# Performance work log

Hardware: AMD Instinct MI355X
Metric: run time of the kernel (lower is better)

## Reference

```python
import jax, jax.numpy as jnp
import numpy as np

B, N, DIM, HEADS = 8, 512, 512, 16
MAX_DIST, NG = 128, 32
RBF_STOP = 20.0
EPS = 1e-5


def _ln(x, g, b):
    m = jnp.mean(x, axis=-1, keepdims=True)
    v = jnp.mean((x - m) ** 2, axis=-1, keepdims=True)
    return (x - m) * jax.lax.rsqrt(v + EPS) * g + b


def setup_inputs() -> dict:
    key = jax.random.key(0)
    ks = jax.random.split(key, 12)
    d = DIM
    s = 0.02
    return {
        "x": jax.random.normal(ks[0], (B * N, d), jnp.float32),
        "dist_matrix": jax.random.randint(ks[1], (B, N, N), 0, MAX_DIST, jnp.int32),
        "dist_3d": jax.random.uniform(ks[2], (B, N, N), jnp.float32) * RBF_STOP,
        "norm1_g": jnp.ones((d,), jnp.float32),
        "norm1_b": jnp.zeros((d,), jnp.float32),
        "in_proj_w": jax.random.normal(ks[3], (3 * d, d), jnp.float32) * s,
        "in_proj_b": jnp.zeros((3 * d,), jnp.float32),
        "out_proj_w": jax.random.normal(ks[4], (d, d), jnp.float32) * s,
        "out_proj_b": jnp.zeros((d,), jnp.float32),
        "dist_emb": jax.random.normal(ks[5], (MAX_DIST, HEADS), jnp.float32) * s,
        "rbf_w": jax.random.normal(ks[6], (HEADS, NG), jnp.float32) * s,
        "rbf_b": jnp.zeros((HEADS,), jnp.float32),
        "norm2_g": jnp.ones((d,), jnp.float32),
        "norm2_b": jnp.zeros((d,), jnp.float32),
        "ffn_w1": jax.random.normal(ks[7], (4 * d, d), jnp.float32) * s,
        "ffn_b1": jnp.zeros((4 * d,), jnp.float32),
        "ffn_w2": jax.random.normal(ks[8], (d, 4 * d), jnp.float32) * s,
        "ffn_b2": jnp.zeros((d,), jnp.float32),
        "batch": jnp.repeat(jnp.arange(B, dtype=jnp.int32), N),
    }


def reference(x, dist_matrix, dist_3d, norm1_g, norm1_b, in_proj_w, in_proj_b,
              out_proj_w, out_proj_b, dist_emb, rbf_w, rbf_b, norm2_g, norm2_b,
              ffn_w1, ffn_b1, ffn_w2, ffn_b2, batch):
    b, n = dist_matrix.shape[0], dist_matrix.shape[1]
    d = x.shape[-1]
    dh = d // HEADS
    # equal-size graphs -> to_dense_batch is a reshape, mask all-true
    xd = x.reshape(b, n, d)

    # additive attention bias: shortest-path-distance embedding + RBF projection
    dc = jnp.clip(dist_matrix, 0, MAX_DIST - 1)
    bias_spd = dist_emb[dc]                                  # [b, n, n, H]
    offset = jnp.linspace(0.0, RBF_STOP, NG, dtype=jnp.float32)
    coeff = -0.5 / (RBF_STOP / (NG - 1)) ** 2
    rbf = jnp.exp(coeff * (dist_3d[..., None] - offset) ** 2)  # [b, n, n, NG]
    bias_3d = rbf @ rbf_w.T + rbf_b                          # [b, n, n, H]
    bias = jnp.transpose(bias_spd + bias_3d, (0, 3, 1, 2))   # [b, H, n, n]

    # multi-head attention (pre-norm residual, as in source)
    h = _ln(xd, norm1_g, norm1_b)
    qkv = h @ in_proj_w.T + in_proj_b
    q, k, v = jnp.split(qkv, 3, axis=-1)
    q = q.reshape(b, n, HEADS, dh).transpose(0, 2, 1, 3)
    k = k.reshape(b, n, HEADS, dh).transpose(0, 2, 1, 3)
    v = v.reshape(b, n, HEADS, dh).transpose(0, 2, 1, 3)
    scores = jnp.einsum('bhqd,bhkd->bhqk', q, k) / jnp.sqrt(jnp.float32(dh)) + bias
    attn = jax.nn.softmax(scores, axis=-1)
    ctx = jnp.einsum('bhqk,bhkd->bhqd', attn, v)
    ctx = ctx.transpose(0, 2, 1, 3).reshape(b, n, d)
    attn_out = ctx @ out_proj_w.T + out_proj_b
    h = h + attn_out

    # FFN (dropout inactive at eval)
    h2 = _ln(h, norm2_g, norm2_b)
    ff = jax.nn.gelu(h2 @ ffn_w1.T + ffn_b1, approximate=False) @ ffn_w2.T + ffn_b2
    h = h + ff
    return h.reshape(b * n, d)
```

## Files before the change

### kernel.cpp

```cpp
#include <hip/hip_runtime.h>
#include <hip/hip_bf16.h>
#include <math.h>

#define BB 8
#define NN 512
#define DD 512
#define NH 16
#define DH 32
#define TD 1536
#define NG 32
#define MAXD 128

typedef __attribute__((ext_vector_type(8))) short bf16x8;
typedef __attribute__((ext_vector_type(4))) float f32x4;

__device__ inline short f2bf(float x) {
    __hip_bfloat16 h = __float2bfloat16(x);
    return *reinterpret_cast<short*>(&h);
}
__device__ inline float bf2f(short x) {
    union { unsigned u; float f; } c;
    c.u = ((unsigned)(unsigned short)x) << 16;
    return c.f;
}

__device__ inline void gld_lds16(const void* g, void* l) {
    __builtin_amdgcn_global_load_lds(
        (const __attribute__((address_space(1))) unsigned int*)g,
        (__attribute__((address_space(3))) unsigned int*)l, 16, 0, 0);
}

__global__ __launch_bounds__(256) void cvt_weights(
    const float* __restrict__ s0, const float* __restrict__ s1,
    const float* __restrict__ s2, const float* __restrict__ s3,
    short* __restrict__ d0, short* __restrict__ d1,
    short* __restrict__ d2, short* __restrict__ d3,
    const float* __restrict__ rbfw, const float* __restrict__ rbfb,
    short* __restrict__ Tg,
    int n0, int n1, int n2, int n3) {
    if (blockIdx.y == 4) {
        if (blockIdx.x != 0) return;
        const float STEP  = 20.0f / 31.0f;
        const float COEFF = -0.5f / (STEP * STEP);
        for (int idx = threadIdx.x; idx < 194 * 16; idx += 256) {
            const int i = idx >> 4, h = idx & 15;
            const float x = fminf((float)i, 192.0f) * (20.0f / 192.0f);
            float acc = rbfb[h];
#pragma unroll
            for (int g = 0; g < NG; g++) {
                const float t = x - (float)g * STEP;
                acc += __expf(COEFF * t * t) * rbfw[h * NG + g];
            }
            Tg[idx] = f2bf(acc);
        }
        return;
    }
    const float* s; short* d; int n;
    switch (blockIdx.y) {
        case 0: s = s0; d = d0; n = n0; break;
        case 1: s = s1; d = d1; n = n1; break;
        case 2: s = s2; d = d2; n = n2; break;
        default: s = s3; d = d3; n = n3; break;
    }
    const int i = (blockIdx.x * 256 + threadIdx.x) * 4;
    if (i >= n) return;
    const float4 v = *(const float4*)(s + i);
    short4 o;
    o.x = f2bf(v.x); o.y = f2bf(v.y); o.z = f2bf(v.z); o.w = f2bf(v.w);
    *(short4*)(d + i) = o;
}

__global__ __launch_bounds__(256) void ln_kernel(const float* __restrict__ x,
                                                 const float* __restrict__ g,
                                                 const float* __restrict__ b,
                                                 short* __restrict__ out_bf) {
    const int row = blockIdx.x;
    const int tid = threadIdx.x;
    const int wave = tid >> 6, lane = tid & 63;
    const float* xr = x + (size_t)row * DD;
    const float v0 = xr[tid], v1 = xr[tid + 256];
    float s = v0 + v1, q = v0 * v0 + v1 * v1;
#pragma unroll
    for (int m = 1; m < 64; m <<= 1) { s += __shfl_xor(s, m); q += __shfl_xor(q, m); }
    __shared__ float ps[8];
    if (lane == 0) { ps[wave] = s; ps[wave + 4] = q; }
    __syncthreads();
    s = ps[0] + ps[1] + ps[2] + ps[3];
    q = ps[4] + ps[5] + ps[6] + ps[7];
    const float mean = s * (1.0f / DD);
    const float var  = q * (1.0f / DD) - mean * mean;
    const float rs   = rsqrtf(var + 1e-5f);
    out_bf[(size_t)row * DD + tid]       = f2bf((v0 - mean) * rs * g[tid] + b[tid]);
    out_bf[(size_t)row * DD + tid + 256] = f2bf((v1 - mean) * rs * g[tid + 256] + b[tid + 256]);
}

template <int TM, bool GELU, bool RES, bool OUTBF>
__global__ __launch_bounds__(256) void gemm_bf16(
    const short* __restrict__ A, const short* __restrict__ Bw,
    const float* __restrict__ bias, const float* __restrict__ res,
    void* __restrict__ Cout, int M, int Nout, int K) {
    const int MI = TM / 32;
    const int bm = blockIdx.y * TM;
    const int bn = blockIdx.x * 128;
    const int tid  = threadIdx.x;
    const int wave = tid >> 6;
    const int lane = tid & 63;
    const int l16  = lane & 15;
    const int quad = lane >> 4;
    const int wr = (wave >> 1) * (TM / 2);
    const int wc = (wave & 1) * 64;

    __shared__ short As[2][TM * 32];
    __shared__ short Bs[2][128 * 32];

    f32x4 acc[MI][4];
#pragma unroll
    for (int i = 0; i < MI; i++)
#pragma unroll
        for (int j = 0; j < 4; j++) acc[i][j] = (f32x4){0.f, 0.f, 0.f, 0.f};

    auto stage = [&](int buf, int k0) {
        const short* Ab = A + (size_t)bm * K + k0;
        const short* Bb = Bw + (size_t)bn * K + k0;
#pragma unroll
        for (int j = 0; j < TM / 64; j++) {
            const int idx = j * 256 + wave * 64 + lane;
            gld_lds16(Ab + (size_t)(idx >> 2) * K + (idx & 3) * 8,
                      &As[buf][(size_t)(j * 256 + wave * 64) * 8]);
        }
#pragma unroll
        for (int j = 0; j < 2; j++) {
            const int idx = j * 256 + wave * 64 + lane;
            gld_lds16(Bb + (size_t)(idx >> 2) * K + (idx & 3) * 8,
                      &Bs[buf][(size_t)(j * 256 + wave * 64) * 8]);
        }
    };
    auto compute = [&](int buf) {
        bf16x8 af[MI], bfr[4];
#pragma unroll
        for (int i = 0; i < MI; i++)
            af[i] = *(const bf16x8*)&As[buf][(wr + i * 16 + l16) * 32 + quad * 8];
#pragma unroll
        for (int j = 0; j < 4; j++)
            bfr[j] = *(const bf16x8*)&Bs[buf][(wc + j * 16 + l16) * 32 + quad * 8];
#pragma unroll
        for (int i = 0; i < MI; i++)
#pragma unroll
            for (int j = 0; j < 4; j++)
                acc[i][j] = __builtin_amdgcn_mfma_f32_16x16x32_bf16(af[i], bfr[j], acc[i][j], 0, 0, 0);
    };

    stage(0, 0);
    __syncthreads();
    int cur = 0;
    for (int k0 = 32; k0 < K; k0 += 32) {
        stage(cur ^ 1, k0);
        compute(cur);
        __syncthreads();
        cur ^= 1;
    }
    compute(cur);

#pragma unroll
    for (int i = 0; i < MI; i++) {
#pragma unroll
        for (int r = 0; r < 4; r++) {
            const int row = bm + wr + i * 16 + quad * 4 + r;
#pragma unroll
            for (int j = 0; j < 4; j++) {
                const int col = bn + wc + j * 16 + l16;
                float v = acc[i][j][r] + bias[col];
                if (GELU) v = 0.5f * v * (1.0f + erff(v * 0.70710678118654752f));
                if (RES)  v += res[(size_t)row * Nout + col];
                if (OUTBF) ((short*)Cout)[(size_t)row * Nout + col] = f2bf(v);
                else       ((float*)Cout)[(size_t)row * Nout + col] = v;
            }
        }
    }
}

__global__ __launch_bounds__(256) void gemm_op(
    const short* __restrict__ Opart,
    const float* __restrict__ lpart,
    const short* __restrict__ Bw,
    const float* __restrict__ bias,
    const short* __restrict__ resb,
    float* __restrict__ Cout) {
    const int bm = blockIdx.y * 64;
    const int bn = blockIdx.x * 128;
    const int tid  = threadIdx.x;
    const int wave = tid >> 6;
    const int lane = tid & 63;
    const int l16  = lane & 15;
    const int quad = lane >> 4;
    const int wr = (wave >> 1) * 32;
    const int wc = (wave & 1) * 64;
    const size_t PO = (size_t)4096 * 512;

    __shared__ short As[2][64 * 32];
    __shared__ short Bs[2][128 * 32];
    __shared__ float Lr[64 * 16];

    for (int i = tid; i < 64 * 16; i += 256) {
        const int idx = (bm + (i >> 4)) * 16 + (i & 15);
        Lr[i] = 1.0f / (lpart[idx] + lpart[4096 * 16 + idx] + lpart[2 * 4096 * 16 + idx]);
    }
    __syncthreads();

    f32x4 acc[2][4];
#pragma unroll
    for (int i = 0; i < 2; i++)
#pragma unroll
        for (int j = 0; j < 4; j++) acc[i][j] = (f32x4){0.f, 0.f, 0.f, 0.f};

    const int arow = tid >> 2;
    const int acb  = (tid & 3) * 8;

    auto stageA = [&](int buf, int k0) {
        const size_t base = (size_t)(bm + arow) * 512 + k0 + acb;
        const bf16x8 a0 = *(const bf16x8*)(Opart + base);
        const bf16x8 a1 = *(const bf16x8*)(Opart + PO + base);
        const bf16x8 a2 = *(const bf16x8*)(Opart + 2 * PO + base);
        const float rv = Lr[arow * 16 + (k0 >> 5)];
        bf16x8 o;
#pragma unroll
        for (int e = 0; e < 8; e++)
            o[e] = f2bf((bf2f(a0[e]) + bf2f(a1[e]) + bf2f(a2[e])) * rv);
        *(bf16x8*)&As[buf][arow * 32 + acb] = o;
    };
    auto stageB = [&](int buf, int k0) {
        const short* Bb = Bw + (size_t)bn * 512 + k0;
#pragma unroll
        for (int j = 0; j < 2; j++) {
            const int idx = j * 256 + wave * 64 + lane;
            gld_lds16(Bb + (size_t)(idx >> 2) * 512 + (idx & 3) * 8,
                      &Bs[buf][(size_t)(j * 256 + wave * 64) * 8]);
        }
    };
    auto compute = [&](int buf) {
        bf16x8 af[2], bfr[4];
#pragma unroll
        for (int i = 0; i < 2; i++)
            af[i] = *(const bf16x8*)&As[buf][(wr + i * 16 + l16) * 32 + quad * 8];
#pragma unroll
        for (int j = 0; j < 4; j++)
            bfr[j] = *(const bf16x8*)&Bs[buf][(wc + j * 16 + l16) * 32 + quad * 8];
#pragma unroll
        for (int i = 0; i < 2; i++)
#pragma unroll
            for (int j = 0; j < 4; j++)
                acc[i][j] = __builtin_amdgcn_mfma_f32_16x16x32_bf16(af[i], bfr[j], acc[i][j], 0, 0, 0);
    };

    stageB(0, 0);
    stageA(0, 0);
    __syncthreads();
    int cur = 0;
    for (int k0 = 32; k0 < 512; k0 += 32) {
        stageB(cur ^ 1, k0);
        stageA(cur ^ 1, k0);
        compute(cur);
        __syncthreads();
        cur ^= 1;
    }
    compute(cur);

#pragma unroll
    for (int i = 0; i < 2; i++) {
#pragma unroll
        for (int r = 0; r < 4; r++) {
            const int row = bm + wr + i * 16 + quad * 4 + r;
#pragma unroll
            for (int j = 0; j < 4; j++) {
                const int col = bn + wc + j * 16 + l16;
                float v = acc[i][j][r] + bias[col] + bf2f(resb[(size_t)row * 512 + col]);
                Cout[(size_t)row * 512 + col] = v;
            }
        }
    }
}

__global__ __launch_bounds__(512) void attn_mfma(
    const short* __restrict__ qkv,
    const int* __restrict__ dist,
    const float* __restrict__ dist3d,
    const float* __restrict__ demb,
    const short* __restrict__ Tg,
    short* __restrict__ O_part,
    float* __restrict__ l_part)
{
    const int blk  = blockIdx.x;
    const int b    = blk & 7;
    const int t3   = blk >> 3;
    const int part = t3 % 3;
    const int q0   = (t3 / 3) * 16;
    const int tid  = threadIdx.x;
    const int wave = tid >> 6;
    const int lane = tid & 63;
    const int l16  = lane & 15;
    const int quad = lane >> 4;

    __shared__ short Kc[NH * 16 * 32];
    __shared__ short Vc[NH * 16 * 32];
    __shared__ short Pb[8 * 16 * 32];
    __shared__ short Tt[194 * 18];
    __shared__ short Db[128 * 18];

    for (int i = tid; i < 8 * 16 * 32; i += 512) Pb[i] = 0;
    for (int i = tid; i < 194 * 16; i += 512) Tt[(i >> 4) * 18 + (i & 15)] = Tg[i];
    for (int i = tid; i < 128 * 16; i += 512) Db[(i >> 4) * 18 + (i & 15)] = f2bf(demb[i]);

    const float scale = 0.17677669529663687f;
    bf16x8 qf[2];
#pragma unroll
    for (int h = 0; h < 2; h++) {
        const int hh = wave * 2 + h;
        qf[h] = *(const bf16x8*)(qkv + (size_t)(b * NN + q0 + l16) * TD + hh * DH + quad * 8);
    }

    f32x4 O[2][2];
    float lsum[2][4];
#pragma unroll
    for (int h = 0; h < 2; h++) {
#pragma unroll
        for (int tt = 0; tt < 2; tt++) O[h][tt] = (f32x4){0.f, 0.f, 0.f, 0.f};
#pragma unroll
        for (int r = 0; r < 4; r++) lsum[h][r] = 0.f;
    }

    __syncthreads();

    const int cbeg = part * 11;
    const int cend = (part == 2) ? 32 : cbeg + 11;

    const int sk = lane >> 2;
    const int sc = lane & 3;

    for (int c = cbeg; c < cend; c++) {
        const int k0 = c * 16;
        const size_t rowb = (size_t)(b * NN + k0 + sk) * TD + sc * 8;
#pragma unroll
        for (int h = 0; h < 2; h++) {
            const int hh = wave * 2 + h;
            gld_lds16(qkv + rowb + DD + hh * DH,     &Kc[hh * 512]);
            gld_lds16(qkv + rowb + 2 * DD + hh * DH, &Vc[hh * 512]);
        }
        float biasr[2][4];
        {
            const int hh0 = wave * 2, hh1 = hh0 + 1;
#pragma unroll
            for (int r = 0; r < 4; r++) {
                const size_t off = ((size_t)(b * NN) + q0 + quad * 4 + r) * NN + k0 + l16;
                int dc = dist[off];
                dc = min(max(dc, 0), MAXD - 1);
                int ii = (int)(dist3d[off] * 9.6f + 0.5f);
                ii = min(ii, 192);
                biasr[0][r] = bf2f(Db[dc * 18 + hh0]) + bf2f(Tt[ii * 18 + hh0]);
                biasr[1][r] = bf2f(Db[dc * 18 + hh1]) + bf2f(Tt[ii * 18 + hh1]);
            }
        }
        asm volatile("" ::: "memory");
        __builtin_amdgcn_s_waitcnt(0x0F70);
        asm volatile("" ::: "memory");
#pragma unroll
        for (int h = 0; h < 2; h++) {
            const int hh = wave * 2 + h;
            const bf16x8 kf = *(const bf16x8*)&Kc[hh * 512 + l16 * 32 + quad * 8];
            f32x4 s = __builtin_amdgcn_mfma_f32_16x16x32_bf16(
                qf[h], kf, (f32x4){0.f, 0.f, 0.f, 0.f}, 0, 0, 0);
            float pv[4];
#pragma unroll
            for (int r = 0; r < 4; r++) {
                float sv = s[r] * scale + biasr[h][r];
                sv = fminf(sv, 20.f);
                pv[r] = __expf(sv);
                lsum[h][r] += pv[r];
                Pb[wave * 512 + (quad * 4 + r) * 32 + l16] = f2bf(pv[r]);
            }
            const bf16x8 pf = *(const bf16x8*)&Pb[wave * 512 + l16 * 32 + quad * 8];
#pragma unroll
            for (int tt = 0; tt < 2; tt++) {
                bf16x8 vf;
                if (quad < 2) {
#pragma unroll
                    for (int j = 0; j < 8; j++)
                        vf[j] = Vc[hh * 512 + (quad * 8 + j) * 32 + tt * 16 + l16];
                } else {
#pragma unroll
                    for (int j = 0; j < 8; j++) vf[j] = 0;
                }
                O[h][tt] = __builtin_amdgcn_mfma_f32_16x16x32_bf16(pf, vf, O[h][tt], 0, 0, 0);
            }
        }
        asm volatile("" ::: "memory");
        __builtin_amdgcn_s_waitcnt(0xC07F);
        asm volatile("" ::: "memory");
    }
    const size_t poff = (size_t)part * 4096;
#pragma unroll
    for (int h = 0; h < 2; h++) {
        const int hh = wave * 2 + h;
#pragma unroll
        for (int m = 1; m < 16; m <<= 1)
#pragma unroll
            for (int r = 0; r < 4; r++) lsum[h][r] += __shfl_xor(lsum[h][r], m);
#pragma unroll
        for (int r = 0; r < 4; r++) {
            const size_t row = (size_t)(b * NN + q0 + quad * 4 + r);
#pragma unroll
            for (int tt = 0; tt < 2; tt++)
                O_part[(poff + row) * DD + hh * DH + tt * 16 + l16] = f2bf(O[h][tt][r]);
            if (l16 == 0) l_part[(poff + row) * NH + hh] = lsum[h][r];
        }
    }
}

extern "C" void kernel_launch(void* const* d_in, const int* in_sizes, int n_in,
                              void* d_out, int out_size, void* d_ws, size_t ws_size,
                              hipStream_t stream) {
    const float* x      = (const float*)d_in[0];
    const int*   dist   = (const int*)d_in[1];
    const float* dist3d = (const float*)d_in[2];
    const float* n1g    = (const float*)d_in[3];
    const float* n1b    = (const float*)d_in[4];
    const float* win    = (const float*)d_in[5];
    const float* bin    = (const float*)d_in[6];
    const float* wo     = (const float*)d_in[7];
    const float* bo     = (const float*)d_in[8];
    const float* demb   = (const float*)d_in[9];
    const float* rbfw   = (const float*)d_in[10];
    const float* rbfb   = (const float*)d_in[11];
    const float* n2g    = (const float*)d_in[12];
    const float* n2b    = (const float*)d_in[13];
    const float* w1     = (const float*)d_in[14];
    const float* b1     = (const float*)d_in[15];
    const float* w2     = (const float*)d_in[16];
    const float* b2     = (const float*)d_in[17];

    char* p = (char*)d_ws;
    short* h_bf   = (short*)p; p += (size_t)4096 * 512 * 2;
    short* qkv_bf = (short*)p; p += (size_t)4096 * 1536 * 2;
    float* hres   = (float*)p; p += (size_t)4096 * 512 * 4;
    short* h2_bf  = (short*)p; p += (size_t)4096 * 512 * 2;
    short* win_bf = (short*)p; p += (size_t)1536 * 512 * 2;
    short* wo_bf  = (short*)p; p += (size_t)512 * 512 * 2;
    short* w1_bf  = (short*)p; p += (size_t)2048 * 512 * 2;
    short* w2_bf  = (short*)p; p += (size_t)512 * 2048 * 2;
    short* Tg     = (short*)p; p += (size_t)8192;
    short* O_part = (short*)p;
    short* mid_bf = (short*)p;
    p += (size_t)4096 * 2048 * 2;
    float* l_part = (float*)p; p += (size_t)3 * 4096 * 16 * 4;

    const int M = BB * NN;

    cvt_weights<<<dim3(1024, 5), 256, 0, stream>>>(
        win, wo, w1, w2, win_bf, wo_bf, w1_bf, w2_bf, rbfw, rbfb, Tg,
        1536 * 512, 512 * 512, 2048 * 512, 512 * 2048);
    ln_kernel<<<M, 256, 0, stream>>>(x, n1g, n1b, h_bf);
    gemm_bf16<64, false, false, true><<<dim3(12, 64), 256, 0, stream>>>(
        h_bf, win_bf, bin, nullptr, qkv_bf, M, TD, DD);
    attn_mfma<<<768, 512, 0, stream>>>(
        qkv_bf, dist, dist3d, demb, Tg, O_part, l_part);
    gemm_op<<<dim3(4, 64), 256, 0, stream>>>(
        O_part, l_part, wo_bf, bo, h_bf, hres);
    ln_kernel<<<M, 256, 0, stream>>>(hres, n2g, n2b, h2_bf);
    gemm_bf16<64, true, false, true><<<dim3(16, 64), 256, 0, stream>>>(
        h2_bf, w1_bf, b1, nullptr, mid_bf, M, 2048, DD);
    gemm_bf16<64, false, true, false><<<dim3(4, 64), 256, 0, stream>>>(
        mid_bf, w2_bf, b2, hres, (float*)d_out, M, DD, 2048);
}
```

Baseline: 252.3 us.

## Double-buffer V, prefetch K to registers, precompute bias indices in attention kernel

The attention kernel now double-buffers V in LDS and prefetches K straight into registers for the next chunk, so loads overlap with compute. The per-chunk dist/dist3d global reads move into a prologue that packs both bias indices into a 16-bit LDS table. V fragments are read with ds_read_b64_tr_b16 transposed loads instead of scalar LDS gathers, the P buffer is padded against bank conflicts, and setprio is raised around the MFMAs. Separately, the QKV and FFN1 GEMMs switch to 128-row tiles, which halves their grid size and may reduce occupancy.

```diff
diff --git a/kernel.cpp b/kernel.cpp
--- a/kernel.cpp
+++ b/kernel.cpp
@@ -13,6 +13,8 @@
 
 typedef __attribute__((ext_vector_type(8))) short bf16x8;
 typedef __attribute__((ext_vector_type(4))) float f32x4;
+typedef __attribute__((ext_vector_type(2))) unsigned int u32x2;
+typedef __attribute__((ext_vector_type(4))) unsigned int u32x4;
 
 __device__ inline short f2bf(float x) {
     __hip_bfloat16 h = __float2bfloat16(x);
@@ -280,7 +282,7 @@
     }
 }
 
-__global__ __launch_bounds__(512) void attn_mfma(
+__global__ __launch_bounds__(512, 4) void attn_mfma(
     const short* __restrict__ qkv,
     const int* __restrict__ dist,
     const float* __restrict__ dist3d,
@@ -299,24 +301,40 @@
     const int lane = tid & 63;
     const int l16  = lane & 15;
     const int quad = lane >> 4;
-
-    __shared__ short Kc[NH * 16 * 32];
-    __shared__ short Vc[NH * 16 * 32];
-    __shared__ short Pb[8 * 16 * 32];
+    const int hh0  = wave * 2;
+
+    const int cbeg = part * 11;
+    const int cend = (part == 2) ? 32 : cbeg + 11;
+    const int kbeg = cbeg * 16;
+    const int kcnt = (cend - cbeg) * 16;
+
+    __shared__ short Vc[2][NH * 16 * 32];
+    __shared__ short Pb[8 * 16 * 40];
     __shared__ short Tt[194 * 18];
     __shared__ short Db[128 * 18];
-
-    for (int i = tid; i < 8 * 16 * 32; i += 512) Pb[i] = 0;
+    __shared__ unsigned short Pk[16 * 178];
+
+    for (int i = tid; i < 8 * 16 * 40; i += 512) Pb[i] = 0;
     for (int i = tid; i < 194 * 16; i += 512) Tt[(i >> 4) * 18 + (i & 15)] = Tg[i];
     for (int i = tid; i < 128 * 16; i += 512) Db[(i >> 4) * 18 + (i & 15)] = f2bf(demb[i]);
+    {
+        const int q  = tid >> 5;
+        const int kl = tid & 31;
+        const size_t rb = ((size_t)(b * NN) + q0 + q) * NN + kbeg;
+        for (int k = kl; k < kcnt; k += 32) {
+            int dc = dist[rb + k];
+            dc = min(max(dc, 0), MAXD - 1);
+            int ii = (int)(dist3d[rb + k] * 9.6f + 0.5f);
+            ii = min(ii, 192);
+            Pk[q * 178 + k] = (unsigned short)(dc | (ii << 8));
+        }
+    }
 
     const float scale = 0.17677669529663687f;
     bf16x8 qf[2];
 #pragma unroll
-    for (int h = 0; h < 2; h++) {
-        const int hh = wave * 2 + h;
-        qf[h] = *(const bf16x8*)(qkv + (size_t)(b * NN + q0 + l16) * TD + hh * DH + quad * 8);
-    }
+    for (int h = 0; h < 2; h++)
+        qf[h] = *(const bf16x8*)(qkv + (size_t)(b * NN + q0 + l16) * TD + (hh0 + h) * DH + quad * 8);
 
     f32x4 O[2][2];
     float lsum[2][4];
@@ -330,44 +348,87 @@
 
     __syncthreads();
 
-    const int cbeg = part * 11;
-    const int cend = (part == 2) ? 32 : cbeg + 11;
-
     const int sk = lane >> 2;
     const int sc = lane & 3;
 
+    auto stageV = [&](int buf, int c) {
+        const size_t rowb = (size_t)(b * NN + c * 16 + sk) * TD + 2 * DD + sc * 8;
+#pragma unroll
+        for (int h = 0; h < 2; h++)
+            gld_lds16(qkv + rowb + (hh0 + h) * DH, &Vc[buf][(hh0 + h) * 512]);
+    };
+    auto loadK = [&](int c, bf16x8* kd) {
+#pragma unroll
+        for (int h = 0; h < 2; h++)
+            kd[h] = *(const bf16x8*)(qkv + (size_t)(b * NN + c * 16 + l16) * TD + DD + (hh0 + h) * DH + quad * 8);
+    };
+
+    bf16x8 kf[2], kfn[2];
+    stageV(0, cbeg);
+    loadK(cbeg, kf);
+    int cur = 0;
+
     for (int c = cbeg; c < cend; c++) {
-        const int k0 = c * 16;
-        const size_t rowb = (size_t)(b * NN + k0 + sk) * TD + sc * 8;
-#pragma unroll
-        for (int h = 0; h < 2; h++) {
-            const int hh = wave * 2 + h;
-            gld_lds16(qkv + rowb + DD + hh * DH,     &Kc[hh * 512]);
-            gld_lds16(qkv + rowb + 2 * DD + hh * DH, &Vc[hh * 512]);
-        }
-        float biasr[2][4];
-        {
-            const int hh0 = wave * 2, hh1 = hh0 + 1;
-#pragma unroll
-            for (int r = 0; r < 4; r++) {
-                const size_t off = ((size_t)(b * NN) + q0 + quad * 4 + r) * NN + k0 + l16;
-                int dc = dist[off];
-                dc = min(max(dc, 0), MAXD - 1);
-                int ii = (int)(dist3d[off] * 9.6f + 0.5f);
-                ii = min(ii, 192);
-                biasr[0][r] = bf2f(Db[dc * 18 + hh0]) + bf2f(Tt[ii * 18 + hh0]);
-                biasr[1][r] = bf2f(Db[dc * 18 + hh1]) + bf2f(Tt[ii * 18 + hh1]);
-            }
-        }
         asm volatile("" ::: "memory");
         __builtin_amdgcn_s_waitcnt(0x0F70);
         asm volatile("" ::: "memory");
+        if (c + 1 < cend) {
+            stageV(cur ^ 1, c + 1);
+            loadK(c + 1, kfn);
+        }
+
+        float biasr[2][4];
+#pragma unroll
+        for (int r = 0; r < 4; r++) {
+            const unsigned u  = Pk[(quad * 4 + r) * 178 + (c - cbeg) * 16 + l16];
+            const unsigned dc = u & 0xFFu;
+            const unsigned ii = u >> 8;
+            const unsigned du = *(const unsigned*)&Db[dc * 18 + hh0];
+            const unsigned tu = *(const unsigned*)&Tt[ii * 18 + hh0];
+            union { unsigned x; float f; } a0, a1, b0, b1;
+            a0.x = du << 16; a1.x = du & 0xFFFF0000u;
+            b0.x = tu << 16; b1.x = tu & 0xFFFF0000u;
+            biasr[0][r] = a0.f + b0.f;
+            biasr[1][r] = a1.f + b1.f;
+        }
+
+        u32x2 raw[2][4];
+        if (quad < 2) {
+#pragma unroll
+            for (int h = 0; h < 2; h++) {
+                const unsigned va =
+                    (unsigned)(uintptr_t)&Vc[cur][(hh0 + h) * 512 + quad * 256 + l16];
+#pragma unroll
+                for (int r = 0; r < 4; r++)
+                    asm volatile("ds_read_b64_tr_b16 %0, %1 offset:%2"
+                                 : "=v"(raw[h][r]) : "v"(va), "n"(r * 128));
+            }
+        }
+        asm volatile("s_waitcnt lgkmcnt(0)" ::: "memory");
+        __builtin_amdgcn_sched_barrier(0);
+
+        bf16x8 vfr[2][2] = {};
+        if (quad < 2) {
+#pragma unroll
+            for (int h = 0; h < 2; h++) {
+                u32x4 w0, w1;
+#pragma unroll
+                for (int r = 0; r < 4; r++) {
+                    w0[r] = __builtin_amdgcn_perm(raw[h][r].y, raw[h][r].x, 0x05040100u);
+                    w1[r] = __builtin_amdgcn_perm(raw[h][r].y, raw[h][r].x, 0x07060302u);
+                }
+                union { u32x4 u; bf16x8 s; } cv0, cv1;
+                cv0.u = w0; cv1.u = w1;
+                vfr[h][0] = cv0.s;
+                vfr[h][1] = cv1.s;
+            }
+        }
+
+        __builtin_amdgcn_s_setprio(1);
 #pragma unroll
         for (int h = 0; h < 2; h++) {
-            const int hh = wave * 2 + h;
-            const bf16x8 kf = *(const bf16x8*)&Kc[hh * 512 + l16 * 32 + quad * 8];
             f32x4 s = __builtin_amdgcn_mfma_f32_16x16x32_bf16(
-                qf[h], kf, (f32x4){0.f, 0.f, 0.f, 0.f}, 0, 0, 0);
+                qf[h], kf[h], (f32x4){0.f, 0.f, 0.f, 0.f}, 0, 0, 0);
             float pv[4];
 #pragma unroll
             for (int r = 0; r < 4; r++) {
@@ -375,31 +436,22 @@
                 sv = fminf(sv, 20.f);
                 pv[r] = __expf(sv);
                 lsum[h][r] += pv[r];
-                Pb[wave * 512 + (quad * 4 + r) * 32 + l16] = f2bf(pv[r]);
+                Pb[wave * 640 + (quad * 4 + r) * 40 + l16] = f2bf(pv[r]);
             }
-            const bf16x8 pf = *(const bf16x8*)&Pb[wave * 512 + l16 * 32 + quad * 8];
-#pragma unroll
-            for (int tt = 0; tt < 2; tt++) {
-                bf16x8 vf;
-                if (quad < 2) {
-#pragma unroll
-                    for (int j = 0; j < 8; j++)
-                        vf[j] = Vc[hh * 512 + (quad * 8 + j) * 32 + tt * 16 + l16];
-                } else {
-#pragma unroll
-                    for (int j = 0; j < 8; j++) vf[j] = 0;
-                }
-                O[h][tt] = __builtin_amdgcn_mfma_f32_16x16x32_bf16(pf, vf, O[h][tt], 0, 0, 0);
-            }
-        }
-        asm volatile("" ::: "memory");
-        __builtin_amdgcn_s_waitcnt(0xC07F);
-        asm volatile("" ::: "memory");
-    }
+            const bf16x8 pf = *(const bf16x8*)&Pb[wave * 640 + l16 * 40 + quad * 8];
+            O[h][0] = __builtin_amdgcn_mfma_f32_16x16x32_bf16(pf, vfr[h][0], O[h][0], 0, 0, 0);
+            O[h][1] = __builtin_amdgcn_mfma_f32_16x16x32_bf16(pf, vfr[h][1], O[h][1], 0, 0, 0);
+        }
+        __builtin_amdgcn_s_setprio(0);
+
+        kf[0] = kfn[0]; kf[1] = kfn[1];
+        cur ^= 1;
+    }
+
     const size_t poff = (size_t)part * 4096;
 #pragma unroll
     for (int h = 0; h < 2; h++) {
-        const int hh = wave * 2 + h;
+        const int hh = hh0 + h;
 #pragma unroll
         for (int m = 1; m < 16; m <<= 1)
 #pragma unroll
@@ -458,14 +510,14 @@
         win, wo, w1, w2, win_bf, wo_bf, w1_bf, w2_bf, rbfw, rbfb, Tg,
         1536 * 512, 512 * 512, 2048 * 512, 512 * 2048);
     ln_kernel<<<M, 256, 0, stream>>>(x, n1g, n1b, h_bf);
-    gemm_bf16<64, false, false, true><<<dim3(12, 64), 256, 0, stream>>>(
+    gemm_bf16<128, false, false, true><<<dim3(12, 32), 256, 0, stream>>>(
         h_bf, win_bf, bin, nullptr, qkv_bf, M, TD, DD);
     attn_mfma<<<768, 512, 0, stream>>>(
         qkv_bf, dist, dist3d, demb, Tg, O_part, l_part);
     gemm_op<<<dim3(4, 64), 256, 0, stream>>>(
         O_part, l_part, wo_bf, bo, h_bf, hres);
     ln_kernel<<<M, 256, 0, stream>>>(hres, n2g, n2b, h2_bf);
-    gemm_bf16<64, true, false, true><<<dim3(16, 64), 256, 0, stream>>>(
+    gemm_bf16<128, true, false, true><<<dim3(16, 32), 256, 0, stream>>>(
         h2_bf, w1_bf, b1, nullptr, mid_bf, M, 2048, DD);
     gemm_bf16<64, false, true, false><<<dim3(4, 64), 256, 0, stream>>>(
         mid_bf, w2_bf, b2, hres, (float*)d_out, M, DD, 2048);
```

Measured after the change: 250.4 us. About the same (-0.7%).

## Rewrite attention kernel without key split, transposed LDS reads, exp2 and packed bias

Applied to the files above, without the earlier changes.

The attention kernel no longer splits keys into three partitions. Each block now walks all 512 keys in 32-key chunks, normalises by the row sum itself and writes bf16 output directly, so the partial buffers and the custom gemm_op merge kernel are removed and the generic GEMM with a bf16 residual does the output projection. Inside attention, the clipped distance and RBF indices are precomputed into packed LDS entries. K is loaded into registers with prefetch, V is double-buffered and read with ds_read_b64_tr_b16 transposed LDS reads, and exp2 with log2e-prescaled bias and scale replaces expf. The QKV and FFN1 GEMMs also move to 128-row tiles. The result is fewer blocks (256) with far more LDS per block, which trades parallelism and occupancy for less partial-sum traffic and one fewer kernel launch.

```diff
diff --git a/kernel.cpp b/kernel.cpp
--- a/kernel.cpp
+++ b/kernel.cpp
@@ -13,6 +13,8 @@
 
 typedef __attribute__((ext_vector_type(8))) short bf16x8;
 typedef __attribute__((ext_vector_type(4))) float f32x4;
+typedef __attribute__((ext_vector_type(2))) unsigned int u32x2;
+typedef __attribute__((ext_vector_type(4))) unsigned int u32x4;
 
 __device__ inline short f2bf(float x) {
     __hip_bfloat16 h = __float2bfloat16(x);
@@ -22,6 +24,16 @@
     union { unsigned u; float f; } c;
     c.u = ((unsigned)(unsigned short)x) << 16;
     return c.f;
+}
+__device__ inline unsigned cvt_pk_bf16(float lo, float hi) {
+    unsigned r;
+    asm("v_cvt_pk_bf16_f32 %0, %1, %2" : "=v"(r) : "v"(lo), "v"(hi));
+    return r;
+}
+__device__ inline float exp2fast(float x) {
+    float r;
+    asm("v_exp_f32 %0, %1" : "=v"(r) : "v"(x));
+    return r;
 }
 
 __device__ inline void gld_lds16(const void* g, void* l) {
@@ -51,7 +63,7 @@
                 const float t = x - (float)g * STEP;
                 acc += __expf(COEFF * t * t) * rbfw[h * NG + g];
             }
-            Tg[idx] = f2bf(acc);
+            Tg[idx] = f2bf(acc * 1.44269504088896f);
         }
         return;
     }
@@ -94,10 +106,10 @@
     out_bf[(size_t)row * DD + tid + 256] = f2bf((v1 - mean) * rs * g[tid + 256] + b[tid + 256]);
 }
 
-template <int TM, bool GELU, bool RES, bool OUTBF>
+template <int TM, bool GELU, int RESMODE, bool OUTBF>
 __global__ __launch_bounds__(256) void gemm_bf16(
     const short* __restrict__ A, const short* __restrict__ Bw,
-    const float* __restrict__ bias, const float* __restrict__ res,
+    const float* __restrict__ bias, const void* __restrict__ res,
     void* __restrict__ Cout, int M, int Nout, int K) {
     const int MI = TM / 32;
     const int bm = blockIdx.y * TM;
@@ -171,7 +183,8 @@
                 const int col = bn + wc + j * 16 + l16;
                 float v = acc[i][j][r] + bias[col];
                 if (GELU) v = 0.5f * v * (1.0f + erff(v * 0.70710678118654752f));
-                if (RES)  v += res[(size_t)row * Nout + col];
+                if (RESMODE == 1) v += ((const float*)res)[(size_t)row * Nout + col];
+                if (RESMODE == 2) v += bf2f(((const short*)res)[(size_t)row * Nout + col]);
                 if (OUTBF) ((short*)Cout)[(size_t)row * Nout + col] = f2bf(v);
                 else       ((float*)Cout)[(size_t)row * Nout + col] = v;
             }
@@ -179,144 +192,50 @@
     }
 }
 
-__global__ __launch_bounds__(256) void gemm_op(
-    const short* __restrict__ Opart,
-    const float* __restrict__ lpart,
-    const short* __restrict__ Bw,
-    const float* __restrict__ bias,
-    const short* __restrict__ resb,
-    float* __restrict__ Cout) {
-    const int bm = blockIdx.y * 64;
-    const int bn = blockIdx.x * 128;
+__global__ __launch_bounds__(512, 2) void attn_mfma(
+    const short* __restrict__ qkv,
+    const int* __restrict__ dist,
+    const float* __restrict__ dist3d,
+    const float* __restrict__ demb,
+    const short* __restrict__ Tg,
+    short* __restrict__ Obf) {
+    const int blk  = blockIdx.x;
+    const int b    = blk & 7;
+    const int q0   = (blk >> 3) * 16;
     const int tid  = threadIdx.x;
     const int wave = tid >> 6;
     const int lane = tid & 63;
     const int l16  = lane & 15;
     const int quad = lane >> 4;
-    const int wr = (wave >> 1) * 32;
-    const int wc = (wave & 1) * 64;
-    const size_t PO = (size_t)4096 * 512;
-
-    __shared__ short As[2][64 * 32];
-    __shared__ short Bs[2][128 * 32];
-    __shared__ float Lr[64 * 16];
-
-    for (int i = tid; i < 64 * 16; i += 256) {
-        const int idx = (bm + (i >> 4)) * 16 + (i & 15);
-        Lr[i] = 1.0f / (lpart[idx] + lpart[4096 * 16 + idx] + lpart[2 * 4096 * 16 + idx]);
-    }
-    __syncthreads();
-
-    f32x4 acc[2][4];
-#pragma unroll
-    for (int i = 0; i < 2; i++)
-#pragma unroll
-        for (int j = 0; j < 4; j++) acc[i][j] = (f32x4){0.f, 0.f, 0.f, 0.f};
-
-    const int arow = tid >> 2;
-    const int acb  = (tid & 3) * 8;
-
-    auto stageA = [&](int buf, int k0) {
-        const size_t base = (size_t)(bm + arow) * 512 + k0 + acb;
-        const bf16x8 a0 = *(const bf16x8*)(Opart + base);
-        const bf16x8 a1 = *(const bf16x8*)(Opart + PO + base);
-        const bf16x8 a2 = *(const bf16x8*)(Opart + 2 * PO + base);
-        const float rv = Lr[arow * 16 + (k0 >> 5)];
-        bf16x8 o;
-#pragma unroll
-        for (int e = 0; e < 8; e++)
-            o[e] = f2bf((bf2f(a0[e]) + bf2f(a1[e]) + bf2f(a2[e])) * rv);
-        *(bf16x8*)&As[buf][arow * 32 + acb] = o;
-    };
-    auto stageB = [&](int buf, int k0) {
-        const short* Bb = Bw + (size_t)bn * 512 + k0;
-#pragma unroll
-        for (int j = 0; j < 2; j++) {
-            const int idx = j * 256 + wave * 64 + lane;
-            gld_lds16(Bb + (size_t)(idx >> 2) * 512 + (idx & 3) * 8,
-                      &Bs[buf][(size_t)(j * 256 + wave * 64) * 8]);
-        }
-    };
-    auto compute = [&](int buf) {
-        bf16x8 af[2], bfr[4];
-#pragma unroll
-        for (int i = 0; i < 2; i++)
-            af[i] = *(const bf16x8*)&As[buf][(wr + i * 16 + l16) * 32 + quad * 8];
-#pragma unroll
-        for (int j = 0; j < 4; j++)
-            bfr[j] = *(const bf16x8*)&Bs[buf][(wc + j * 16 + l16) * 32 + quad * 8];
-#pragma unroll
-        for (int i = 0; i < 2; i++)
-#pragma unroll
-            for (int j = 0; j < 4; j++)
-                acc[i][j] = __builtin_amdgcn_mfma_f32_16x16x32_bf16(af[i], bfr[j], acc[i][j], 0, 0, 0);
-    };
-
-    stageB(0, 0);
-    stageA(0, 0);
-    __syncthreads();
-    int cur = 0;
-    for (int k0 = 32; k0 < 512; k0 += 32) {
-        stageB(cur ^ 1, k0);
-        stageA(cur ^ 1, k0);
-        compute(cur);
-        __syncthreads();
-        cur ^= 1;
-    }
-    compute(cur);
-
-#pragma unroll
-    for (int i = 0; i < 2; i++) {
-#pragma unroll
-        for (int r = 0; r < 4; r++) {
-            const int row = bm + wr + i * 16 + quad * 4 + r;
-#pragma unroll
-            for (int j = 0; j < 4; j++) {
-                const int col = bn + wc + j * 16 + l16;
-                float v = acc[i][j][r] + bias[col] + bf2f(resb[(size_t)row * 512 + col]);
-                Cout[(size_t)row * 512 + col] = v;
-            }
-        }
-    }
-}
-
-__global__ __launch_bounds__(512) void attn_mfma(
-    const short* __restrict__ qkv,
-    const int* __restrict__ dist,
-    const float* __restrict__ dist3d,
-    const float* __restrict__ demb,
-    const short* __restrict__ Tg,
-    short* __restrict__ O_part,
-    float* __restrict__ l_part)
-{
-    const int blk  = blockIdx.x;
-    const int b    = blk & 7;
-    const int t3   = blk >> 3;
-    const int part = t3 % 3;
-    const int q0   = (t3 / 3) * 16;
-    const int tid  = threadIdx.x;
-    const int wave = tid >> 6;
-    const int lane = tid & 63;
-    const int l16  = lane & 15;
-    const int quad = lane >> 4;
-
-    __shared__ short Kc[NH * 16 * 32];
-    __shared__ short Vc[NH * 16 * 32];
-    __shared__ short Pb[8 * 16 * 32];
+    const int hh0  = wave * 2;
+
+    __shared__ short Vc[2][NH * 1024];
+    __shared__ short Pb[16 * 512];
     __shared__ short Tt[194 * 18];
     __shared__ short Db[128 * 18];
-
-    for (int i = tid; i < 8 * 16 * 32; i += 512) Pb[i] = 0;
+    __shared__ unsigned short Pk[512 * 16];
+
     for (int i = tid; i < 194 * 16; i += 512) Tt[(i >> 4) * 18 + (i & 15)] = Tg[i];
-    for (int i = tid; i < 128 * 16; i += 512) Db[(i >> 4) * 18 + (i & 15)] = f2bf(demb[i]);
-
-    const float scale = 0.17677669529663687f;
+    for (int i = tid; i < 128 * 16; i += 512)
+        Db[(i >> 4) * 18 + (i & 15)] = f2bf(demb[i] * 1.44269504088896f);
+    {
+        const size_t rb = ((size_t)(b * NN) + q0) * NN;
+#pragma unroll
+        for (int q = 0; q < 16; q++) {
+            const size_t off = rb + (size_t)q * NN + tid;
+            int dc = dist[off];
+            dc = min(max(dc, 0), MAXD - 1);
+            int ii = (int)(dist3d[off] * 9.6f + 0.5f);
+            ii = min(ii, 192);
+            Pk[tid * 16 + q] = (unsigned short)(dc | (ii << 8));
+        }
+    }
+
+    const float scale = 0.17677669529663687f * 1.44269504088896f;
     bf16x8 qf[2];
 #pragma unroll
-    for (int h = 0; h < 2; h++) {
-        const int hh = wave * 2 + h;
-        qf[h] = *(const bf16x8*)(qkv + (size_t)(b * NN + q0 + l16) * TD + hh * DH + quad * 8);
-    }
+    for (int h = 0; h < 2; h++)
+        qf[h] = *(const bf16x8*)(qkv + (size_t)(b * NN + q0 + l16) * TD + (hh0 + h) * DH + quad * 8);
 
     f32x4 O[2][2];
     float lsum[2][4];
@@ -330,87 +249,141 @@
 
     __syncthreads();
 
-    const int cbeg = part * 11;
-    const int cend = (part == 2) ? 32 : cbeg + 11;
-
     const int sk = lane >> 2;
     const int sc = lane & 3;
 
-    for (int c = cbeg; c < cend; c++) {
-        const int k0 = c * 16;
-        const size_t rowb = (size_t)(b * NN + k0 + sk) * TD + sc * 8;
+    auto stageV = [&](int buf, int c) {
+        const size_t rowb = (size_t)(b * NN + c * 32 + sk) * TD + 2 * DD + sc * 8;
 #pragma unroll
         for (int h = 0; h < 2; h++) {
-            const int hh = wave * 2 + h;
-            gld_lds16(qkv + rowb + DD + hh * DH,     &Kc[hh * 512]);
-            gld_lds16(qkv + rowb + 2 * DD + hh * DH, &Vc[hh * 512]);
-        }
-        float biasr[2][4];
-        {
-            const int hh0 = wave * 2, hh1 = hh0 + 1;
-#pragma unroll
-            for (int r = 0; r < 4; r++) {
-                const size_t off = ((size_t)(b * NN) + q0 + quad * 4 + r) * NN + k0 + l16;
-                int dc = dist[off];
-                dc = min(max(dc, 0), MAXD - 1);
-                int ii = (int)(dist3d[off] * 9.6f + 0.5f);
-                ii = min(ii, 192);
-                biasr[0][r] = bf2f(Db[dc * 18 + hh0]) + bf2f(Tt[ii * 18 + hh0]);
-                biasr[1][r] = bf2f(Db[dc * 18 + hh1]) + bf2f(Tt[ii * 18 + hh1]);
-            }
-        }
+            short* dst = &Vc[buf][(hh0 + h) * 1024];
+            gld_lds16(qkv + rowb + (hh0 + h) * DH, dst);
+            gld_lds16(qkv + rowb + (size_t)16 * TD + (hh0 + h) * DH, dst + 512);
+        }
+    };
+    auto loadK = [&](int c, bf16x8 (*kd)[2]) {
+#pragma unroll
+        for (int h = 0; h < 2; h++) {
+            const short* base =
+                qkv + (size_t)(b * NN + c * 32 + l16) * TD + DD + (hh0 + h) * DH + quad * 8;
+            kd[h][0] = *(const bf16x8*)base;
+            kd[h][1] = *(const bf16x8*)(base + 16 * TD);
+        }
+    };
+
+    bf16x8 kf[2][2], kfn[2][2];
+    stageV(0, 0);
+    loadK(0, kf);
+    int cur = 0;
+
+    for (int c = 0; c < 16; c++) {
         asm volatile("" ::: "memory");
         __builtin_amdgcn_s_waitcnt(0x0F70);
         asm volatile("" ::: "memory");
+
+        u32x2 vraw[2][4];
 #pragma unroll
         for (int h = 0; h < 2; h++) {
-            const int hh = wave * 2 + h;
-            const bf16x8 kf = *(const bf16x8*)&Kc[hh * 512 + l16 * 32 + quad * 8];
-            f32x4 s = __builtin_amdgcn_mfma_f32_16x16x32_bf16(
-                qf[h], kf, (f32x4){0.f, 0.f, 0.f, 0.f}, 0, 0, 0);
-            float pv[4];
+            const unsigned va =
+                (unsigned)(uintptr_t)&Vc[cur][(hh0 + h) * 1024 + quad * 128 + l16];
+            asm volatile("ds_read_b64_tr_b16 %0, %1 offset:0"    : "=v"(vraw[h][0]) : "v"(va));
+            asm volatile("ds_read_b64_tr_b16 %0, %1 offset:128"  : "=v"(vraw[h][1]) : "v"(va));
+            asm volatile("ds_read_b64_tr_b16 %0, %1 offset:1024" : "=v"(vraw[h][2]) : "v"(va));
+            asm volatile("ds_read_b64_tr_b16 %0, %1 offset:1152" : "=v"(vraw[h][3]) : "v"(va));
+        }
+
+        if (c + 1 < 16) {
+            stageV(cur ^ 1, c + 1);
+            loadK(c + 1, kfn);
+        }
+
+#pragma unroll
+        for (int half = 0; half < 2; half++) {
+            const ushort4 pk4 =
+                *(const ushort4*)&Pk[(unsigned)((c * 32 + half * 16 + l16) * 16 + quad * 4)];
+            const unsigned short pe[4] = {pk4.x, pk4.y, pk4.z, pk4.w};
+            float bb[2][4];
 #pragma unroll
             for (int r = 0; r < 4; r++) {
-                float sv = s[r] * scale + biasr[h][r];
-                sv = fminf(sv, 20.f);
-                pv[r] = __expf(sv);
-                lsum[h][r] += pv[r];
-                Pb[wave * 512 + (quad * 4 + r) * 32 + l16] = f2bf(pv[r]);
+                const unsigned u  = pe[r];
+                const unsigned dc = u & 0xFFu;
+                const unsigned ii = u >> 8;
+                const unsigned du = *(const unsigned*)&Db[dc * 18 + hh0];
+                const unsigned tu = *(const unsigned*)&Tt[ii * 18 + hh0];
+                union { unsigned x; float f; } a0, a1, b0, b1;
+                a0.x = du << 16; a1.x = du & 0xFFFF0000u;
+                b0.x = tu << 16; b1.x = tu & 0xFFFF0000u;
+                bb[0][r] = a0.f + b0.f;
+                bb[1][r] = a1.f + b1.f;
             }
-            const bf16x8 pf = *(const bf16x8*)&Pb[wave * 512 + l16 * 32 + quad * 8];
-#pragma unroll
-            for (int tt = 0; tt < 2; tt++) {
-                bf16x8 vf;
-                if (quad < 2) {
-#pragma unroll
-                    for (int j = 0; j < 8; j++)
-                        vf[j] = Vc[hh * 512 + (quad * 8 + j) * 32 + tt * 16 + l16];
-                } else {
-#pragma unroll
-                    for (int j = 0; j < 8; j++) vf[j] = 0;
+#pragma unroll
+            for (int h = 0; h < 2; h++) {
+                f32x4 s = __builtin_amdgcn_mfma_f32_16x16x32_bf16(
+                    qf[h], kf[h][half], (f32x4){0.f, 0.f, 0.f, 0.f}, 0, 0, 0);
+                float pv[4];
+#pragma unroll
+                for (int r = 0; r < 4; r++) {
+                    float sv = s[r] * scale + bb[h][r];
+                    sv = fminf(sv, 28.853901f);
+                    pv[r] = exp2fast(sv);
+                    lsum[h][r] += pv[r];
                 }
-                O[h][tt] = __builtin_amdgcn_mfma_f32_16x16x32_bf16(pf, vf, O[h][tt], 0, 0, 0);
+                u32x2 w;
+                w[0] = cvt_pk_bf16(pv[0], pv[1]);
+                w[1] = cvt_pk_bf16(pv[2], pv[3]);
+                *(u32x2*)&Pb[(wave * 2 + h) * 512 + (half * 16 + l16) * 16 + quad * 4] = w;
             }
         }
+
         asm volatile("" ::: "memory");
-        __builtin_amdgcn_s_waitcnt(0xC07F);
-        asm volatile("" ::: "memory");
-    }
-    const size_t poff = (size_t)part * 4096;
+        asm volatile("s_waitcnt lgkmcnt(0)" ::: "memory");
+        __builtin_amdgcn_sched_barrier(0);
+
+        u32x2 praw[2][2];
+#pragma unroll
+        for (int h = 0; h < 2; h++) {
+            const unsigned pa =
+                (unsigned)(uintptr_t)&Pb[(wave * 2 + h) * 512 + quad * 64 + l16];
+            asm volatile("ds_read_b64_tr_b16 %0, %1 offset:0"   : "=v"(praw[h][0]) : "v"(pa));
+            asm volatile("ds_read_b64_tr_b16 %0, %1 offset:512" : "=v"(praw[h][1]) : "v"(pa));
+        }
+        asm volatile("s_waitcnt lgkmcnt(0)" ::: "memory");
+        __builtin_amdgcn_sched_barrier(0);
+
+        __builtin_amdgcn_s_setprio(1);
+#pragma unroll
+        for (int h = 0; h < 2; h++) {
+            union { u32x4 u; bf16x8 s; } pf, v0, v1;
+            pf.u = (u32x4){praw[h][0][0], praw[h][0][1], praw[h][1][0], praw[h][1][1]};
+#pragma unroll
+            for (int r = 0; r < 4; r++) {
+                v0.u[r] = __builtin_amdgcn_perm(vraw[h][r][1], vraw[h][r][0], 0x05040100u);
+                v1.u[r] = __builtin_amdgcn_perm(vraw[h][r][1], vraw[h][r][0], 0x07060302u);
+            }
+            O[h][0] = __builtin_amdgcn_mfma_f32_16x16x32_bf16(pf.s, v0.s, O[h][0], 0, 0, 0);
+            O[h][1] = __builtin_amdgcn_mfma_f32_16x16x32_bf16(pf.s, v1.s, O[h][1], 0, 0, 0);
+        }
+        __builtin_amdgcn_s_setprio(0);
+
+#pragma unroll
+        for (int h = 0; h < 2; h++) { kf[h][0] = kfn[h][0]; kf[h][1] = kfn[h][1]; }
+        cur ^= 1;
+    }
+
 #pragma unroll
     for (int h = 0; h < 2; h++) {
-        const int hh = wave * 2 + h;
+        const int hh = hh0 + h;
 #pragma unroll
         for (int m = 1; m < 16; m <<= 1)
 #pragma unroll
             for (int r = 0; r < 4; r++) lsum[h][r] += __shfl_xor(lsum[h][r], m);
 #pragma unroll
         for (int r = 0; r < 4; r++) {
+            const float rl = 1.0f / lsum[h][r];
             const size_t row = (size_t)(b * NN + q0 + quad * 4 + r);
 #pragma unroll
             for (int tt = 0; tt < 2; tt++)
-                O_part[(poff + row) * DD + hh * DH + tt * 16 + l16] = f2bf(O[h][tt][r]);
-            if (l16 == 0) l_part[(poff + row) * NH + hh] = lsum[h][r];
+                Obf[row * DD + hh * DH + tt * 16 + l16] = f2bf(O[h][tt][r] * rl);
         }
     }
 }
@@ -447,10 +420,9 @@
     short* w1_bf  = (short*)p; p += (size_t)2048 * 512 * 2;
     short* w2_bf  = (short*)p; p += (size_t)512 * 2048 * 2;
     short* Tg     = (short*)p; p += (size_t)8192;
-    short* O_part = (short*)p;
+    short* o_bf   = (short*)p;
     short* mid_bf = (short*)p;
     p += (size_t)4096 * 2048 * 2;
-    float* l_part = (float*)p; p += (size_t)3 * 4096 * 16 * 4;
 
     const int M = BB * NN;
 
@@ -458,15 +430,15 @@
         win, wo, w1, w2, win_bf, wo_bf, w1_bf, w2_bf, rbfw, rbfb, Tg,
         1536 * 512, 512 * 512, 2048 * 512, 512 * 2048);
     ln_kernel<<<M, 256, 0, stream>>>(x, n1g, n1b, h_bf);
-    gemm_bf16<64, false, false, true><<<dim3(12, 64), 256, 0, stream>>>(
+    gemm_bf16<128, false, 0, true><<<dim3(12, 32), 256, 0, stream>>>(
         h_bf, win_bf, bin, nullptr, qkv_bf, M, TD, DD);
-    attn_mfma<<<768, 512, 0, stream>>>(
-        qkv_bf, dist, dist3d, demb, Tg, O_part, l_part);
-    gemm_op<<<dim3(4, 64), 256, 0, stream>>>(
-        O_part, l_part, wo_bf, bo, h_bf, hres);
+    attn_mfma<<<256, 512, 0, stream>>>(
+        qkv_bf, dist, dist3d, demb, Tg, o_bf);
+    gemm_bf16<64, false, 2, false><<<dim3(4, 64), 256, 0, stream>>>(
+        o_bf, wo_bf, bo, h_bf, hres, M, DD, DD);
     ln_kernel<<<M, 256, 0, stream>>>(hres, n2g, n2b, h2_bf);
-    gemm_bf16<64, true, false, true><<<dim3(16, 64), 256, 0, stream>>>(
+    gemm_bf16<128, true, 0, true><<<dim3(16, 32), 256, 0, stream>>>(
         h2_bf, w1_bf, b1, nullptr, mid_bf, M, 2048, DD);
-    gemm_bf16<64, false, true, false><<<dim3(4, 64), 256, 0, stream>>>(
+    gemm_bf16<64, false, 1, false><<<dim3(4, 64), 256, 0, stream>>>(
         mid_bf, w2_bf, b2, hres, (float*)d_out, M, DD, 2048);
 }
```

Measured after the change: 239.4 us. -5.1%, faster.
